# Optimization experiments

Hardware: AMD Instinct MI355X
Metric: run time of the kernel (lower is better)

The kernel has to match this reference:

```python
import jax, jax.numpy as jnp
import numpy as np
import itertools

EPS = 1e-3  # BatchNorm1d eps in the original module
N_VOX = 100000


def _build_sparse_structure():
    """Build realistic clustered voxel coords, a 3x3x3 submanifold neighbor
    table (spconv rulebook equivalent), and the unique-merge mapping used by
    sum_duplicates. All index structure is constant (non-differentiable)."""
    rng = np.random.default_rng(0)
    B, Z, Y, X = 2, 40, 1600, 1408  # sparse_shape = grid_size[::-1] + [1,0,0]
    offs01 = np.array(list(itertools.product([0, 1], repeat=3)), dtype=np.int64)
    coords = []
    for b in range(B):
        base = np.stack([rng.integers(0, Z - 1, 13000),
                         rng.integers(0, Y - 1, 13000),
                         rng.integers(0, X - 1, 13000)], 1)
        exp = (base[:, None, :] + offs01[None]).reshape(-1, 3)  # clustered voxels
        coords.append(np.concatenate([np.full((len(exp), 1), b, np.int64), exp], 1))
    coords = np.unique(np.concatenate(coords, 0), axis=0)[:N_VOX]
    assert len(coords) == N_VOX
    # lexicographic unique order => encoded keys are sorted ascending
    key = ((coords[:, 0] * Z + coords[:, 1]) * Y + coords[:, 2]) * X + coords[:, 3]
    offs27 = np.array(list(itertools.product([-1, 0, 1], repeat=3)), np.int64)
    nc = coords[:, None, 1:] + offs27[None]  # [N,27,3]
    inb = (nc >= 0).all(-1) & (nc[..., 0] < Z) & (nc[..., 1] < Y) & (nc[..., 2] < X)
    nk = ((coords[:, None, 0] * Z + nc[..., 0]) * Y + nc[..., 1]) * X + nc[..., 2]
    pos = np.searchsorted(key, nk).clip(0, N_VOX - 1)
    valid = inb & (key[pos] == nk)
    nbr_idx = np.where(valid, pos, -1).astype(np.int32)  # [N,27], -1 = empty
    # second sparse tensor: half its voxels coincide, half are shifted in x
    coords2 = coords.copy()
    coords2[::2, 3] = np.minimum(coords2[::2, 3] + 1, X - 1)
    comb = np.concatenate([coords, coords2], 0)
    uniq, inv = np.unique(comb, axis=0, return_inverse=True)
    return nbr_idx, inv.astype(np.int32), int(len(uniq))


def setup_inputs() -> dict:
    nbr_idx, seg_ids, num_segments = _build_sparse_structure()
    key = jax.random.key(0)
    ks = jax.random.split(key, 6)
    C = 16
    return {
        'voxel_features': jax.random.normal(ks[0], (N_VOX, C), jnp.float32),
        'feat2': jax.random.normal(ks[1], (N_VOX, C), jnp.float32),
        'W0': jax.random.normal(ks[2], (27, C, 16), jnp.float32) * 0.1,
        'g0': jnp.ones((16,), jnp.float32),
        'b0': jnp.zeros((16,), jnp.float32),
        'W1': jax.random.normal(ks[3], (27, 16, 16), jnp.float32) * 0.1,
        'g1': jnp.ones((16,), jnp.float32),
        'b1': jnp.zeros((16,), jnp.float32),
        'Wobo': jax.random.normal(ks[4], (16, 16), jnp.float32) * 0.1,
        'bobo': jnp.zeros((16,), jnp.float32),
        'Wf': jax.random.normal(ks[5], (16, 128), jnp.float32) * 0.1,
        'bf': jnp.zeros((128,), jnp.float32),
        'nbr_idx': jnp.asarray(nbr_idx),
        'seg_ids': jnp.asarray(seg_ids),
        'num_segments': num_segments,
    }


def _subm_bn_relu(x, W, g, b, nbr_idx):
    """Submanifold 3x3x3 sparse conv (gather->GEMM) + BatchNorm1d + ReLU."""
    N = x.shape[0]
    xp = jnp.concatenate([x, jnp.zeros((1, x.shape[1]), x.dtype)], 0)  # pad row
    idx = jnp.where(nbr_idx < 0, N, nbr_idx)  # missing neighbor -> zero row
    y = jnp.einsum('nkc,kco->no', xp[idx], W)  # [N,27,Cin] x [27,Cin,Cout]
    mu = y.mean(0)
    var = y.var(0)
    return jax.nn.relu((y - mu) * jax.lax.rsqrt(var + EPS) * g + b)


def reference(voxel_features, feat2, W0, g0, b0, W1, g1, b1, Wobo, bobo, Wf, bf,
              nbr_idx, seg_ids, num_segments):
    # level-0 conv_input + conv1 (subm conv, BN, ReLU)
    h = _subm_bn_relu(voxel_features, W0, g0, b0, nbr_idx)
    h = _subm_bn_relu(h, W1, g1, b1, nbr_idx)
    # obo_* 1x1 sparse conv on the second branch (plain matmul + bias)
    t2 = feat2 @ Wobo + bobo
    # sum_duplicates: merge coincident sparse indices by summing features
    comb = jnp.concatenate([h, t2], 0)  # [2N,16]
    merged = jax.ops.segment_sum(comb, seg_ids, num_segments=num_segments)
    # final 1x1 sparse conv
    return merged @ Wf + bf  # [U,128]
```

## Files before the change

### kernel.cpp

```cpp
#include <hip/hip_runtime.h>

#define BN_EPS 1e-3f
#define STATC  32
#define MBLK   128

using bfrag  = __attribute__((ext_vector_type(8))) short;
using f32x4v = __attribute__((ext_vector_type(4))) float;

__device__ __forceinline__ unsigned short f2bf(float f) {
    union { float f; unsigned u; } v; v.f = f;
    unsigned r = v.u + 0x7FFFu + ((v.u >> 16) & 1u);
    return (unsigned short)(r >> 16);
}

__global__ __launch_bounds__(256)
void prep_kernel(const float* __restrict__ vf,
                 const float* __restrict__ W0, const float* __restrict__ W1,
                 const float* __restrict__ Wf, const int* __restrict__ seg,
                 unsigned short* __restrict__ xb0,
                 unsigned short* __restrict__ Wb0, unsigned short* __restrict__ Wb1,
                 unsigned short* __restrict__ Wfb,
                 float* __restrict__ stats,
                 int* __restrict__ hidx, int* __restrict__ t2s, int N)
{
    int t = blockIdx.x * 256 + threadIdx.x;
    int TA = 2 * (N + 1);
    unsigned short tmp[8];
    if (t < TA) {
        int n = t >> 1, h = t & 1;
        if (n < N) {
            const f32x4v* yr = (const f32x4v*)(vf + (size_t)n * 16 + h * 8);
            f32x4v v0 = __builtin_nontemporal_load(yr);
            f32x4v v1 = __builtin_nontemporal_load(yr + 1);
#pragma unroll
            for (int j = 0; j < 4; ++j) { tmp[j] = f2bf(v0[j]); tmp[4 + j] = f2bf(v1[j]); }
        } else {
#pragma unroll
            for (int j = 0; j < 8; ++j) tmp[j] = 0;
        }
        *(int4*)(xb0 + (size_t)n * 16 + h * 8) = *(int4*)tmp;
        return;
    }
    t -= TA;
    if (t < 2 * 14 * 64) {
        int w = t >= 896;
        int l = t - w * 896;
        int s = l >> 6, lane = l & 63;
        int q = lane >> 4, n = lane & 15;
        int tap = 2 * s + (q >> 1);
        int cb  = (q & 1) * 8;
        const float* W = w ? W1 : W0;
        unsigned short* Wb = w ? Wb1 : Wb0;
#pragma unroll
        for (int j = 0; j < 8; ++j)
            tmp[j] = (tap < 27) ? f2bf(W[((size_t)(tap * 16 + cb + j)) * 16 + n]) : 0;
        *(int4*)(Wb + (size_t)l * 8) = *(int4*)tmp;
        return;
    }
    t -= 2 * 14 * 64;
    if (t < 512) {
        int ct = t >> 6, lane = t & 63;
        int q = lane >> 4, n = lane & 15;
#pragma unroll
        for (int j = 0; j < 8; ++j)
            tmp[j] = (q < 2) ? f2bf(Wf[(size_t)(q * 8 + j) * 128 + ct * 16 + n]) : 0;
        *(int4*)(Wfb + (size_t)t * 8) = *(int4*)tmp;
        return;
    }
    t -= 512;
    if (t < 2 * STATC * 32) { stats[t] = 0.f; return; }
    t -= 2 * STATC * 32;
    if (t < N) { hidx[seg[t]] = t; return; }
    t -= N;
    if (t < N) {
        int s = seg[N + t];
        if (t == 0 || seg[N + t - 1] != s) t2s[s] = t;
    }
}

__global__ __launch_bounds__(256)
void conv_stats_kernel(const unsigned short* __restrict__ xb,
                       const unsigned short* __restrict__ Wb,
                       const int* __restrict__ nbr,
                       float* __restrict__ y,
                       float* __restrict__ statsC,
                       int N)
{
    __shared__ int   sNbr[64 * 27];
    __shared__ float sY[64 * 16];
    __shared__ float sred[32];
    int tid = threadIdx.x;
    if (tid < 32) sred[tid] = 0.f;

    int gb = blockIdx.x * 1728;
    int NT = N * 27;
#pragma unroll
    for (int i = 0; i < 7; ++i) {
        int t = i * 256 + tid;
        if (t < 1728) {
            int g = gb + t;
            sNbr[t] = (g < NT) ? __builtin_nontemporal_load(nbr + g) : -1;
        }
    }
    __syncthreads();

    int lane = tid & 63, wib = tid >> 6;
    int q = lane >> 4, m = lane & 15;
    int c0   = (q & 1) * 8;
    int tpar = q >> 1;
    int lvox = wib * 16 + m;

    int idx[14];
#pragma unroll
    for (int s = 0; s < 14; ++s) {
        int tap = 2 * s + tpar;
        int id  = (tap < 27) ? sNbr[lvox * 27 + tap] : -1;
        idx[s]  = (id >= 0) ? id : N;
    }

    f32x4v acc = {0.f, 0.f, 0.f, 0.f};
#pragma unroll
    for (int s = 0; s < 14; ++s) {
        bfrag a = *(const bfrag*)(xb + (size_t)idx[s] * 16 + c0);
        bfrag b = *(const bfrag*)(Wb + ((size_t)s * 64 + lane) * 8);
        acc = __builtin_amdgcn_mfma_f32_16x16x32_bf16(a, b, acc, 0, 0, 0);
    }

    int o = lane & 15;
#pragma unroll
    for (int i = 0; i < 4; ++i)
        sY[(wib * 16 + q * 4 + i) * 16 + o] = acc[i];

    float s  = acc[0] + acc[1] + acc[2] + acc[3];
    float qq = acc[0] * acc[0] + acc[1] * acc[1] + acc[2] * acc[2] + acc[3] * acc[3];
    s  += __shfl_xor(s, 16);  s  += __shfl_xor(s, 32);
    qq += __shfl_xor(qq, 16); qq += __shfl_xor(qq, 32);
    if (lane < 16) {
        atomicAdd(&sred[lane], s);
        atomicAdd(&sred[16 + lane], qq);
    }
    __syncthreads();

    {
        int row = blockIdx.x * 64 + (tid >> 2);
        if (row < N)
            *(f32x4v*)(y + (size_t)row * 16 + (tid & 3) * 4) =
                *(const f32x4v*)(sY + (size_t)(tid >> 2) * 16 + (tid & 3) * 4);
    }
    if (tid < 32)
        atomicAdd(&statsC[(blockIdx.x & (STATC - 1)) * 32 + tid], sred[tid]);
}

__global__ __launch_bounds__(256)
void bnrelu_cvt_kernel(const float* __restrict__ y0, const float* __restrict__ statsC,
                       const float* __restrict__ g, const float* __restrict__ b,
                       float invN, unsigned short* __restrict__ xb, int N)
{
    __shared__ float sred[32];
    __shared__ float sSc[16], sSh[16];
    int tid = threadIdx.x;
    if (tid < 32) {
        float v = 0.f;
#pragma unroll
        for (int k = 0; k < STATC; ++k) v += statsC[k * 32 + tid];
        sred[tid] = v;
    }
    __syncthreads();
    if (tid < 16) {
        float mu  = sred[tid] * invN;
        float var = sred[16 + tid] * invN - mu * mu;
        float sc  = g[tid] * rsqrtf(var + BN_EPS);
        sSc[tid] = sc;
        sSh[tid] = b[tid] - mu * sc;
    }
    __syncthreads();

    int t = blockIdx.x * 256 + tid;
    if (t >= (N + 1) * 2) return;
    int n = t >> 1, h = t & 1;
    unsigned short tmp[8];
    if (n < N) {
        const f32x4v* yr4 = (const f32x4v*)(y0 + (size_t)n * 16 + h * 8);
        f32x4v v0 = __builtin_nontemporal_load(yr4);
        f32x4v v1 = __builtin_nontemporal_load(yr4 + 1);
#pragma unroll
        for (int j = 0; j < 4; ++j) {
            int c = h * 8 + j;
            tmp[j]     = f2bf(fmaxf(fmaf(v0[j], sSc[c], sSh[c]), 0.f));
            tmp[4 + j] = f2bf(fmaxf(fmaf(v1[j], sSc[c + 4], sSh[c + 4]), 0.f));
        }
    } else {
#pragma unroll
        for (int j = 0; j < 8; ++j) tmp[j] = 0;
    }
    *(int4*)(xb + (size_t)n * 16 + h * 8) = *(int4*)tmp;
}

__global__ __launch_bounds__(256)
void merge_final_kernel(const float* __restrict__ y1, const float* __restrict__ statsC,
                        const float* __restrict__ g, const float* __restrict__ b,
                        float invN,
                        const float* __restrict__ feat2, const float* __restrict__ Wobo,
                        const float* __restrict__ bobo,
                        const int* __restrict__ seg,
                        const int* __restrict__ hidx, const int* __restrict__ t2s,
                        const unsigned short* __restrict__ Wfb,
                        const float* __restrict__ bf,
                        float* __restrict__ out, int N, int U)
{
    __shared__ unsigned short smA[MBLK * 16];
    __shared__ float sred[32];
    __shared__ float sSc[16], sSh[16];
    int tid = threadIdx.x;
    int u0  = blockIdx.x * MBLK;

    if (tid < 32) {
        float v = 0.f;
#pragma unroll
        for (int k = 0; k < STATC; ++k) v += statsC[k * 32 + tid];
        sred[tid] = v;
    }
    __syncthreads();
    if (tid < 16) {
        float mu  = sred[tid] * invN;
        float var = sred[16 + tid] * invN - mu * mu;
        float sc  = g[tid] * rsqrtf(var + BN_EPS);
        sSc[tid] = sc;
        sSh[tid] = b[tid] - mu * sc;
    }
    __syncthreads();

    {
        int sl = tid >> 1, half = tid & 1;
        int u  = u0 + sl;
        bool valid = u < U;
        int uc = valid ? u : 0;
        int hi = hidx[uc];
        int r  = t2s[uc];
        bool hasH = valid && (unsigned)hi < (unsigned)N && seg[hi] == u;
        bool hasT = valid && (unsigned)r  < (unsigned)N && seg[N + r] == u;

        size_t hoff = (size_t)(hasH ? hi : 0) * 16 + half * 8;
        f32x4v yv0 = *(const f32x4v*)(y1 + hoff);
        f32x4v yv1 = *(const f32x4v*)(y1 + hoff + 4);
        size_t toff = (size_t)(hasT ? r : 0) * 16;
        f32x4v f0 = __builtin_nontemporal_load((const f32x4v*)(feat2 + toff));
        f32x4v f1 = __builtin_nontemporal_load((const f32x4v*)(feat2 + toff) + 1);
        f32x4v f2 = __builtin_nontemporal_load((const f32x4v*)(feat2 + toff) + 2);
        f32x4v f3 = __builtin_nontemporal_load((const f32x4v*)(feat2 + toff) + 3);

        float m[8];
#pragma unroll
        for (int j = 0; j < 8; ++j) m[j] = 0.f;
        if (hasH) {
#pragma unroll
            for (int j = 0; j < 4; ++j) {
                int c = half * 8 + j;
                m[j]     = fmaxf(fmaf(yv0[j], sSc[c],     sSh[c]),     0.f);
                m[4 + j] = fmaxf(fmaf(yv1[j], sSc[c + 4], sSh[c + 4]), 0.f);
            }
        }
        if (hasT) {
            float a2[8];
#pragma unroll
            for (int j = 0; j < 8; ++j) a2[j] = bobo[half * 8 + j];
            float fv[16];
            *(f32x4v*)(fv + 0)  = f0; *(f32x4v*)(fv + 4)  = f1;
            *(f32x4v*)(fv + 8)  = f2; *(f32x4v*)(fv + 12) = f3;
            for (;;) {
#pragma unroll
                for (int c = 0; c < 16; ++c) {
                    float xc = fv[c];
                    const float* wr = Wobo + c * 16 + half * 8;
#pragma unroll
                    for (int j = 0; j < 8; ++j) a2[j] = fmaf(xc, wr[j], a2[j]);
                }
                ++r;
                if (r >= N || seg[N + r] != u) break;
                const f32x4v* fr = (const f32x4v*)(feat2 + (size_t)r * 16);
                f32x4v g0 = __builtin_nontemporal_load(fr);
                f32x4v g1 = __builtin_nontemporal_load(fr + 1);
                f32x4v g2 = __builtin_nontemporal_load(fr + 2);
                f32x4v g3 = __builtin_nontemporal_load(fr + 3);
                *(f32x4v*)(fv + 0)  = g0; *(f32x4v*)(fv + 4)  = g1;
                *(f32x4v*)(fv + 8)  = g2; *(f32x4v*)(fv + 12) = g3;
            }
#pragma unroll
            for (int j = 0; j < 8; ++j) m[j] += a2[j];
        }
        unsigned short tb[8];
#pragma unroll
        for (int j = 0; j < 8; ++j) tb[j] = f2bf(m[j]);
        *(int4*)(smA + (size_t)tid * 8) = *(int4*)tb;
    }
    __syncthreads();

    int lane = tid & 63, w = tid >> 6;
    int q = lane >> 4, n = lane & 15;
#pragma unroll
    for (int rt = 0; rt < 2; ++rt) {
        int row0 = w * 32 + rt * 16;
        bfrag a = {0, 0, 0, 0, 0, 0, 0, 0};
        if (q < 2)
            a = *(const bfrag*)(smA + ((size_t)(row0 + n) * 16 + q * 8));
#pragma unroll
        for (int ct = 0; ct < 8; ++ct) {
            bfrag bb = *(const bfrag*)(Wfb + ((size_t)(ct * 64 + lane)) * 8);
            f32x4v acc = {0.f, 0.f, 0.f, 0.f};
            acc = __builtin_amdgcn_mfma_f32_16x16x32_bf16(a, bb, acc, 0, 0, 0);
            int col = ct * 16 + n;
            float bv = bf[col];
#pragma unroll
            for (int i = 0; i < 4; ++i) {
                int u = u0 + row0 + q * 4 + i;
                if (u < U) out[(size_t)u * 128 + col] = acc[i] + bv;
            }
        }
    }
}

extern "C" void kernel_launch(void* const* d_in, const int* in_sizes, int n_in,
                              void* d_out, int out_size, void* d_ws, size_t ws_size,
                              hipStream_t stream)
{
    const float* vf    = (const float*)d_in[0];
    const float* feat2 = (const float*)d_in[1];
    const float* W0    = (const float*)d_in[2];
    const float* g0    = (const float*)d_in[3];
    const float* b0    = (const float*)d_in[4];
    const float* W1    = (const float*)d_in[5];
    const float* g1    = (const float*)d_in[6];
    const float* b1    = (const float*)d_in[7];
    const float* Wobo  = (const float*)d_in[8];
    const float* bobo  = (const float*)d_in[9];
    const float* Wf    = (const float*)d_in[10];
    const float* bf    = (const float*)d_in[11];
    const int*   nbr   = (const int*)d_in[12];
    const int*   seg   = (const int*)d_in[13];

    int N = in_sizes[0] / 16;
    int U = out_size / 128;

    float* out = (float*)d_out;
    float* ws  = (float*)d_ws;

    int gbConv = (N + 63) / 64;

    float* y0     = ws;
    float* y1     = y0 + (size_t)N * 16;
    float* statsA = y1 + (size_t)N * 16;
    float* statsB = statsA + STATC * 32;
    unsigned short* xb0 = (unsigned short*)(statsB + STATC * 32);
    unsigned short* xb1 = xb0 + (size_t)(N + 1) * 16;
    unsigned short* Wb0 = xb1 + (size_t)(N + 1) * 16;
    unsigned short* Wb1 = Wb0 + 14 * 64 * 8;
    unsigned short* Wfb = Wb1 + 14 * 64 * 8;
    int* hidx = (int*)(Wfb + 8 * 64 * 8);
    int* t2s  = hidx + U;

    float invN  = 1.f / (float)N;
    int thrPrep = 2 * (N + 1) + 2 * 14 * 64 + 512 + 2 * STATC * 32 + 2 * N;
    int gbPrep  = (thrPrep + 255) / 256;
    int gbCvt   = ((N + 1) * 2 + 255) / 256;
    int gbMerge = (U + MBLK - 1) / MBLK;

    prep_kernel<<<gbPrep, 256, 0, stream>>>(vf, W0, W1, Wf, seg, xb0, Wb0, Wb1,
                                            Wfb, statsA, hidx, t2s, N);
    conv_stats_kernel<<<gbConv, 256, 0, stream>>>(xb0, Wb0, nbr, y0, statsA, N);
    bnrelu_cvt_kernel<<<gbCvt, 256, 0, stream>>>(y0, statsA, g0, b0, invN, xb1, N);
    conv_stats_kernel<<<gbConv, 256, 0, stream>>>(xb1, Wb1, nbr, y1, statsB, N);
    merge_final_kernel<<<gbMerge, 256, 0, stream>>>(y1, statsB, g1, b1, invN,
                                                    feat2, Wobo, bobo, seg,
                                                    hidx, t2s, Wfb, bf, out, N, U);
}
```

Baseline: 165.0 us.

## Fuse bf16 conversion and BN+ReLU into conv gather, drop separate kernels

Removes the standalone fp32->bf16 input conversion and the BN/ReLU/convert kernel. The conv kernel now gathers fp32 neighbor rows directly and converts them in registers, applying the previous layer's BN affine and ReLU on the fly. The hidx/t2s scatter setup moves into the first conv launch. This saves one launch and the intermediate bf16 buffers, at the cost of gathering twice as many bytes per neighbor (fp32 instead of bf16) and redoing the BN transform for every one of the 27 taps.

```diff
diff --git a/kernel.cpp b/kernel.cpp
--- a/kernel.cpp
+++ b/kernel.cpp
@@ -14,34 +14,14 @@
 }
 
 __global__ __launch_bounds__(256)
-void prep_kernel(const float* __restrict__ vf,
-                 const float* __restrict__ W0, const float* __restrict__ W1,
-                 const float* __restrict__ Wf, const int* __restrict__ seg,
-                 unsigned short* __restrict__ xb0,
+void prep_kernel(const float* __restrict__ W0, const float* __restrict__ W1,
+                 const float* __restrict__ Wf,
                  unsigned short* __restrict__ Wb0, unsigned short* __restrict__ Wb1,
                  unsigned short* __restrict__ Wfb,
-                 float* __restrict__ stats,
-                 int* __restrict__ hidx, int* __restrict__ t2s, int N)
+                 float* __restrict__ stats)
 {
     int t = blockIdx.x * 256 + threadIdx.x;
-    int TA = 2 * (N + 1);
     unsigned short tmp[8];
-    if (t < TA) {
-        int n = t >> 1, h = t & 1;
-        if (n < N) {
-            const f32x4v* yr = (const f32x4v*)(vf + (size_t)n * 16 + h * 8);
-            f32x4v v0 = __builtin_nontemporal_load(yr);
-            f32x4v v1 = __builtin_nontemporal_load(yr + 1);
-#pragma unroll
-            for (int j = 0; j < 4; ++j) { tmp[j] = f2bf(v0[j]); tmp[4 + j] = f2bf(v1[j]); }
-        } else {
-#pragma unroll
-            for (int j = 0; j < 8; ++j) tmp[j] = 0;
-        }
-        *(int4*)(xb0 + (size_t)n * 16 + h * 8) = *(int4*)tmp;
-        return;
-    }
-    t -= TA;
     if (t < 2 * 14 * 64) {
         int w = t >= 896;
         int l = t - w * 896;
@@ -68,29 +48,50 @@
         return;
     }
     t -= 512;
-    if (t < 2 * STATC * 32) { stats[t] = 0.f; return; }
-    t -= 2 * STATC * 32;
-    if (t < N) { hidx[seg[t]] = t; return; }
-    t -= N;
-    if (t < N) {
-        int s = seg[N + t];
-        if (t == 0 || seg[N + t - 1] != s) t2s[s] = t;
-    }
-}
-
+    if (t < 2 * STATC * 32) stats[t] = 0.f;
+}
+
+template<bool BN, bool SCAT>
 __global__ __launch_bounds__(256)
-void conv_stats_kernel(const unsigned short* __restrict__ xb,
-                       const unsigned short* __restrict__ Wb,
-                       const int* __restrict__ nbr,
-                       float* __restrict__ y,
-                       float* __restrict__ statsC,
-                       int N)
+void conv_kernel(const float* __restrict__ xin,
+                 const unsigned short* __restrict__ Wb,
+                 const int* __restrict__ nbr,
+                 const float* __restrict__ statsIn,
+                 const float* __restrict__ g, const float* __restrict__ b,
+                 float invN,
+                 float* __restrict__ y,
+                 float* __restrict__ statsC,
+                 const int* __restrict__ seg,
+                 int* __restrict__ hidx, int* __restrict__ t2s,
+                 int N)
 {
     __shared__ int   sNbr[64 * 27];
     __shared__ float sY[64 * 16];
     __shared__ float sred[32];
+    __shared__ float sSc[16], sSh[16];
     int tid = threadIdx.x;
+
+    if (SCAT) {
+        int t = blockIdx.x * 256 + tid;
+        if (t < N) {
+            hidx[seg[t]] = t;
+        } else if (t < 2 * N) {
+            int r = t - N;
+            int s = seg[N + r];
+            if (r == 0 || seg[N + r - 1] != s) t2s[s] = r;
+        }
+    }
+
     if (tid < 32) sred[tid] = 0.f;
+    if (BN) {
+        if (tid >= 32 && tid < 64) {
+            int c = tid - 32;
+            float v = 0.f;
+#pragma unroll
+            for (int k = 0; k < STATC; ++k) v += statsIn[k * 32 + c];
+            sY[c] = v;
+        }
+    }
 
     int gb = blockIdx.x * 1728;
     int NT = N * 27;
@@ -98,9 +99,17 @@
     for (int i = 0; i < 7; ++i) {
         int t = i * 256 + tid;
         if (t < 1728) {
-            int g = gb + t;
-            sNbr[t] = (g < NT) ? __builtin_nontemporal_load(nbr + g) : -1;
-        }
+            int g2 = gb + t;
+            sNbr[t] = (g2 < NT) ? __builtin_nontemporal_load(nbr + g2) : -1;
+        }
+    }
+    __syncthreads();
+    if (BN && tid < 16) {
+        float mu  = sY[tid] * invN;
+        float var = sY[16 + tid] * invN - mu * mu;
+        float sc  = g[tid] * rsqrtf(var + BN_EPS);
+        sSc[tid] = sc;
+        sSh[tid] = b[tid] - mu * sc;
     }
     __syncthreads();
 
@@ -110,6 +119,12 @@
     int tpar = q >> 1;
     int lvox = wib * 16 + m;
 
+    float scr[8], shr[8];
+    if (BN) {
+#pragma unroll
+        for (int j = 0; j < 8; ++j) { scr[j] = sSc[c0 + j]; shr[j] = sSh[c0 + j]; }
+    }
+
     int idx[14];
 #pragma unroll
     for (int s = 0; s < 14; ++s) {
@@ -121,9 +136,25 @@
     f32x4v acc = {0.f, 0.f, 0.f, 0.f};
 #pragma unroll
     for (int s = 0; s < 14; ++s) {
-        bfrag a = *(const bfrag*)(xb + (size_t)idx[s] * 16 + c0);
-        bfrag b = *(const bfrag*)(Wb + ((size_t)s * 64 + lane) * 8);
-        acc = __builtin_amdgcn_mfma_f32_16x16x32_bf16(a, b, acc, 0, 0, 0);
+        int id  = idx[s];
+        int rid = (id < N) ? id : 0;
+        const f32x4v* p = (const f32x4v*)(xin + (size_t)rid * 16 + c0);
+        f32x4v v0 = p[0], v1 = p[1];
+        unsigned short a8[8];
+        if (BN) {
+#pragma unroll
+            for (int j = 0; j < 4; ++j) {
+                a8[j]     = f2bf(fmaxf(fmaf(v0[j], scr[j],     shr[j]),     0.f));
+                a8[4 + j] = f2bf(fmaxf(fmaf(v1[j], scr[4 + j], shr[4 + j]), 0.f));
+            }
+        } else {
+#pragma unroll
+            for (int j = 0; j < 4; ++j) { a8[j] = f2bf(v0[j]); a8[4 + j] = f2bf(v1[j]); }
+        }
+        bfrag a = *(bfrag*)a8;
+        if (id >= N) a = (bfrag){0, 0, 0, 0, 0, 0, 0, 0};
+        bfrag bb = *(const bfrag*)(Wb + ((size_t)s * 64 + lane) * 8);
+        acc = __builtin_amdgcn_mfma_f32_16x16x32_bf16(a, bb, acc, 0, 0, 0);
     }
 
     int o = lane & 15;
@@ -149,51 +180,6 @@
     }
     if (tid < 32)
         atomicAdd(&statsC[(blockIdx.x & (STATC - 1)) * 32 + tid], sred[tid]);
-}
-
-__global__ __launch_bounds__(256)
-void bnrelu_cvt_kernel(const float* __restrict__ y0, const float* __restrict__ statsC,
-                       const float* __restrict__ g, const float* __restrict__ b,
-                       float invN, unsigned short* __restrict__ xb, int N)
-{
-    __shared__ float sred[32];
-    __shared__ float sSc[16], sSh[16];
-    int tid = threadIdx.x;
-    if (tid < 32) {
-        float v = 0.f;
-#pragma unroll
-        for (int k = 0; k < STATC; ++k) v += statsC[k * 32 + tid];
-        sred[tid] = v;
-    }
-    __syncthreads();
-    if (tid < 16) {
-        float mu  = sred[tid] * invN;
-        float var = sred[16 + tid] * invN - mu * mu;
-        float sc  = g[tid] * rsqrtf(var + BN_EPS);
-        sSc[tid] = sc;
-        sSh[tid] = b[tid] - mu * sc;
-    }
-    __syncthreads();
-
-    int t = blockIdx.x * 256 + tid;
-    if (t >= (N + 1) * 2) return;
-    int n = t >> 1, h = t & 1;
-    unsigned short tmp[8];
-    if (n < N) {
-        const f32x4v* yr4 = (const f32x4v*)(y0 + (size_t)n * 16 + h * 8);
-        f32x4v v0 = __builtin_nontemporal_load(yr4);
-        f32x4v v1 = __builtin_nontemporal_load(yr4 + 1);
-#pragma unroll
-        for (int j = 0; j < 4; ++j) {
-            int c = h * 8 + j;
-            tmp[j]     = f2bf(fmaxf(fmaf(v0[j], sSc[c], sSh[c]), 0.f));
-            tmp[4 + j] = f2bf(fmaxf(fmaf(v1[j], sSc[c + 4], sSh[c + 4]), 0.f));
-        }
-    } else {
-#pragma unroll
-        for (int j = 0; j < 8; ++j) tmp[j] = 0;
-    }
-    *(int4*)(xb + (size_t)n * 16 + h * 8) = *(int4*)tmp;
 }
 
 __global__ __launch_bounds__(256)
@@ -350,25 +336,23 @@
     float* y1     = y0 + (size_t)N * 16;
     float* statsA = y1 + (size_t)N * 16;
     float* statsB = statsA + STATC * 32;
-    unsigned short* xb0 = (unsigned short*)(statsB + STATC * 32);
-    unsigned short* xb1 = xb0 + (size_t)(N + 1) * 16;
-    unsigned short* Wb0 = xb1 + (size_t)(N + 1) * 16;
+    unsigned short* Wb0 = (unsigned short*)(statsB + STATC * 32);
     unsigned short* Wb1 = Wb0 + 14 * 64 * 8;
     unsigned short* Wfb = Wb1 + 14 * 64 * 8;
     int* hidx = (int*)(Wfb + 8 * 64 * 8);
     int* t2s  = hidx + U;
 
     float invN  = 1.f / (float)N;
-    int thrPrep = 2 * (N + 1) + 2 * 14 * 64 + 512 + 2 * STATC * 32 + 2 * N;
-    int gbPrep  = (thrPrep + 255) / 256;
-    int gbCvt   = ((N + 1) * 2 + 255) / 256;
+    int gbPrep  = (2 * 14 * 64 + 512 + 2 * STATC * 32 + 255) / 256;
     int gbMerge = (U + MBLK - 1) / MBLK;
 
-    prep_kernel<<<gbPrep, 256, 0, stream>>>(vf, W0, W1, Wf, seg, xb0, Wb0, Wb1,
-                                            Wfb, statsA, hidx, t2s, N);
-    conv_stats_kernel<<<gbConv, 256, 0, stream>>>(xb0, Wb0, nbr, y0, statsA, N);
-    bnrelu_cvt_kernel<<<gbCvt, 256, 0, stream>>>(y0, statsA, g0, b0, invN, xb1, N);
-    conv_stats_kernel<<<gbConv, 256, 0, stream>>>(xb1, Wb1, nbr, y1, statsB, N);
+    prep_kernel<<<gbPrep, 256, 0, stream>>>(W0, W1, Wf, Wb0, Wb1, Wfb, statsA);
+    conv_kernel<false, true><<<gbConv, 256, 0, stream>>>(
+        vf, Wb0, nbr, nullptr, nullptr, nullptr, 0.f,
+        y0, statsA, seg, hidx, t2s, N);
+    conv_kernel<true, false><<<gbConv, 256, 0, stream>>>(
+        y0, Wb1, nbr, statsA, g0, b0, invN,
+        y1, statsB, seg, nullptr, nullptr, N);
     merge_final_kernel<<<gbMerge, 256, 0, stream>>>(y1, statsB, g1, b1, invN,
                                                     feat2, Wobo, bobo, seg,
                                                     hidx, t2s, Wfb, bf, out, N, U);
```

New measurement: 178.2 us. +8.0%, slower.
